# Kernel optimization log

Hardware: AMD Instinct MI355X
Metric: run time of the kernel (lower is better)

The kernel has to match this reference:

```python
import jax, jax.numpy as jnp
import numpy as np

B = 2000           # number of events (segments)
N = 1_000_000      # total points (sum of num_points)
D_IN, H, D_OUT = 16, 256, 128
EPS = 1e-5


def _layer_norm(x, g, b):
    m = x.mean(-1, keepdims=True)
    v = x.var(-1, keepdims=True)
    return (x - m) * jax.lax.rsqrt(v + EPS) * g + b


def setup_inputs() -> dict:
    key = jax.random.key(0)
    ks = jax.random.split(key, 8)
    # ragged counts, all positive, summing exactly to N
    rng = np.random.default_rng(0)
    counts = np.full(B, N // B, dtype=np.int64)
    d = rng.integers(-400, 401, size=B // 2)
    counts[: B // 2] += d
    counts[B // 2 :] -= d
    assert counts.sum() == N and (counts > 0).all()
    z_t = jax.random.normal(ks[0], (N, D_IN), dtype=jnp.float32)
    def lin(k, fi, fo):
        return jax.random.normal(k, (fi, fo), dtype=jnp.float32) / np.sqrt(fi)
    return {
        "z_t": z_t,
        "W1": lin(ks[1], D_IN, H), "b1": jnp.zeros((H,), jnp.float32),
        "g1": jnp.ones((H,), jnp.float32), "be1": jnp.zeros((H,), jnp.float32),
        "W2": lin(ks[2], H, H), "b2": jnp.zeros((H,), jnp.float32),
        "g2": jnp.ones((H,), jnp.float32), "be2": jnp.zeros((H,), jnp.float32),
        "W3": lin(ks[3], H, D_OUT), "b3": jnp.zeros((D_OUT,), jnp.float32),
        "num_points": jnp.asarray(counts, dtype=jnp.int64),
    }


def reference(z_t, W1, b1, g1, be1, W2, b2, g2, be2, W3, b3, num_points):
    # per-point phi MLP: Linear -> LN -> ReLU (x2) -> Linear
    h = jax.nn.relu(_layer_norm(z_t @ W1 + b1, g1, be1))
    h = jax.nn.relu(_layer_norm(h @ W2 + b2, g2, be2))
    phi = h @ W3 + b3                                  # [N, D_OUT]
    # fused ragged mean-pool + broadcast back (replaces split/stack/repeat_interleave)
    seg = jnp.repeat(jnp.arange(B), num_points, total_repeat_length=N)  # [N]
    sums = jax.ops.segment_sum(phi, seg, num_segments=B)                # [B, D_OUT]
    emb = sums / num_points[:, None].astype(phi.dtype)                  # mean pooling
    return emb[seg]                                                     # [N, D_OUT]
```

## Files before the change

kernel.cpp:

```cpp
#include <hip/hip_runtime.h>
#include <hip/hip_bf16.h>
#include <cstdint>
#include <cstddef>

#define NPTS  1000000
#define BSEG  2000
#define DIN   16
#define HDIM  256
#define DOUT  128
#define NTILE (NPTS / 32)
#define NWG   512

typedef __bf16          bf16x8 __attribute__((ext_vector_type(8)));
typedef unsigned short  us16x8 __attribute__((ext_vector_type(8)));
typedef unsigned int    u32x4  __attribute__((ext_vector_type(4)));
typedef float           f32x4  __attribute__((ext_vector_type(4)));

static __device__ __forceinline__ unsigned short f2bf(float x) {
    unsigned int u = __float_as_uint(x);
    u += 0x7fffu + ((u >> 16) & 1u);
    return (unsigned short)(u >> 16);
}

static __device__ __forceinline__ bf16x8 ldb8(const unsigned short* p) {
    u32x4 v = *(const u32x4*)p;
    return __builtin_bit_cast(bf16x8, v);
}
static __device__ __forceinline__ f32x4 mfma16(bf16x8 a, bf16x8 b, f32x4 c) {
    return __builtin_amdgcn_mfma_f32_16x16x32_bf16(a, b, c, 0, 0, 0);
}
static __device__ __forceinline__ void keep(bf16x8& v) {
    u32x4 u = __builtin_bit_cast(u32x4, v);
    unsigned a0 = u[0], a1 = u[1], a2 = u[2], a3 = u[3];
    asm volatile("" : "+v"(a0), "+v"(a1), "+v"(a2), "+v"(a3));
    u32x4 r; r[0] = a0; r[1] = a1; r[2] = a2; r[3] = a3;
    v = __builtin_bit_cast(bf16x8, r);
}

static __device__ __forceinline__ float rsum16(float x) {
    x += __builtin_bit_cast(float, __builtin_amdgcn_update_dpp(
             0, __builtin_bit_cast(int, x), 0x128, 0xf, 0xf, false));
    x += __builtin_bit_cast(float, __builtin_amdgcn_update_dpp(
             0, __builtin_bit_cast(int, x), 0x124, 0xf, 0xf, false));
    x += __builtin_bit_cast(float, __builtin_amdgcn_update_dpp(
             0, __builtin_bit_cast(int, x), 0x122, 0xf, 0xf, false));
    x += __builtin_bit_cast(float, __builtin_amdgcn_update_dpp(
             0, __builtin_bit_cast(int, x), 0x121, 0xf, 0xf, false));
    return x;
}

__global__ __launch_bounds__(1024) void scan_counts(const int* __restrict__ counts,
                                                    int* __restrict__ offsets) {
    __shared__ int a[2048];
    const int t = threadIdx.x;
    a[t]        = (t        < BSEG) ? counts[t]        : 0;
    a[t + 1024] = (t + 1024 < BSEG) ? counts[t + 1024] : 0;
    for (int s = 1; s < 2048; s <<= 1) {
        __syncthreads();
        int x1 = (t >= s) ? a[t - s] : 0;
        int x2 = a[t + 1024 - s];
        __syncthreads();
        a[t] += x1;
        a[t + 1024] += x2;
    }
    __syncthreads();
    if (t == 0) offsets[0] = 0;
    offsets[t + 1] = a[t];
    if (t + 1024 < BSEG) offsets[t + 1025] = a[t + 1024];
}

__global__ __launch_bounds__(256) void fill_seg(const int* __restrict__ offsets,
                                                unsigned short* __restrict__ seg) {
    const int b  = blockIdx.x;
    const int lo = offsets[b], hi = offsets[b + 1];
    for (int i = lo + threadIdx.x; i < hi; i += 256) seg[i] = (unsigned short)b;
}

__global__ __launch_bounds__(256) void prep_weights(const float* __restrict__ W1,
                                                    const float* __restrict__ W2,
                                                    unsigned short* __restrict__ w1t,
                                                    unsigned short* __restrict__ w2t) {
    const int i = blockIdx.x * 256 + threadIdx.x;
    if (i < HDIM * 32) {
        int n = i >> 5, k = i & 31;
        w1t[i] = (k < DIN) ? f2bf(W1[k * HDIM + n]) : (unsigned short)0;
    } else {
        int j = i - HDIM * 32;
        if (j < HDIM * HDIM) {
            int n = j >> 8, k = j & 255;
            w2t[j] = f2bf(W2[k * HDIM + n]);
        }
    }
}

__global__ __launch_bounds__(256, 2) void fused_phi_pool(
    const float* __restrict__ z,
    const unsigned short* __restrict__ w1t,
    const unsigned short* __restrict__ w2t,
    const float* __restrict__ b1, const float* __restrict__ g1, const float* __restrict__ be1,
    const float* __restrict__ b2, const float* __restrict__ g2, const float* __restrict__ be2,
    const unsigned short* __restrict__ seg,
    float* __restrict__ sums_h) {
    __shared__ __align__(16) unsigned short h1[32][264];
    __shared__ __align__(16) float part[2][32][8];
    __shared__ __align__(16) int seg_sm[2][32];

    const int tid  = threadIdx.x;
    const int wave = tid >> 6;
    const int lane = tid & 63;
    const int l15  = lane & 15;
    const int quad = lane >> 4;
    const int colw = wave * 64 + l15;
    const bool zlane = (quad < 2);

    bf16x8 bw1[4];
    bf16x8 bw2[4][8];
#pragma unroll
    for (int t = 0; t < 4; ++t) {
        const int n = (wave * 4 + t) * 16 + l15;
        bw1[t] = ldb8(w1t + n * 32 + quad * 8);
        keep(bw1[t]);
#pragma unroll
        for (int ks = 0; ks < 8; ++ks) {
            bw2[t][ks] = ldb8(w2t + n * 256 + ks * 32 + quad * 8);
            keep(bw2[t][ks]);
        }
    }
    float b1v[4], g1v[4], e1v[4], b2v[4], g2v[4], e2v[4];
#pragma unroll
    for (int t = 0; t < 4; ++t) {
        const int c = colw + t * 16;
        b1v[t] = b1[c]; g1v[t] = g1[c]; e1v[t] = be1[c];
        b2v[t] = b2[c]; g2v[t] = g2[c]; e2v[t] = be2[c];
    }

    float4 zn[2][2];
    {
        const int base0 = blockIdx.x * 32;
        if (zlane) {
#pragma unroll
            for (int mb = 0; mb < 2; ++mb) {
                const float* zp = z + (size_t)(base0 + mb * 16 + l15) * DIN + quad * 8;
                zn[mb][0] = *(const float4*)zp;
                zn[mb][1] = *(const float4*)(zp + 4);
            }
        }
    }

    int p = 0;
    for (int tile = blockIdx.x; tile < NTILE; tile += NWG, p ^= 1) {
        const int base = tile * 32;
        if (tid < 32) seg_sm[p][tid] = (int)seg[base + tid];

        float4 zc[2][2];
#pragma unroll
        for (int mb = 0; mb < 2; ++mb) { zc[mb][0] = zn[mb][0]; zc[mb][1] = zn[mb][1]; }
        const int ntile = tile + NWG;
        if (zlane && ntile < NTILE) {
            const int nb = ntile * 32;
#pragma unroll
            for (int mb = 0; mb < 2; ++mb) {
                const float* zp = z + (size_t)(nb + mb * 16 + l15) * DIN + quad * 8;
                zn[mb][0] = *(const float4*)zp;
                zn[mb][1] = *(const float4*)(zp + 4);
            }
        }

        f32x4 a1[2][4];
#pragma unroll
        for (int mb = 0; mb < 2; ++mb) {
            bf16x8 af;
            if (zlane) {
                us16x8 u;
                u[0] = f2bf(zc[mb][0].x); u[1] = f2bf(zc[mb][0].y);
                u[2] = f2bf(zc[mb][0].z); u[3] = f2bf(zc[mb][0].w);
                u[4] = f2bf(zc[mb][1].x); u[5] = f2bf(zc[mb][1].y);
                u[6] = f2bf(zc[mb][1].z); u[7] = f2bf(zc[mb][1].w);
                af = __builtin_bit_cast(bf16x8, u);
            } else {
                us16x8 u = {0, 0, 0, 0, 0, 0, 0, 0};
                af = __builtin_bit_cast(bf16x8, u);
            }
            const f32x4 zero = {0.f, 0.f, 0.f, 0.f};
#pragma unroll
            for (int t = 0; t < 4; ++t) a1[mb][t] = mfma16(af, bw1[t], zero);
        }
#pragma unroll
        for (int mb = 0; mb < 2; ++mb) {
            float s[4], q[4];
#pragma unroll
            for (int r = 0; r < 4; ++r) {
                float sv = 0.f, qv = 0.f;
#pragma unroll
                for (int t = 0; t < 4; ++t) {
                    float y = a1[mb][t][r] + b1v[t];
                    a1[mb][t][r] = y;
                    sv += y; qv += y * y;
                }
                s[r] = rsum16(sv); q[r] = rsum16(qv);
            }
            if (l15 == 0) {
#pragma unroll
                for (int r = 0; r < 4; ++r)
                    *(float2*)&part[p][mb * 16 + quad * 4 + r][wave * 2] =
                        make_float2(s[r], q[r]);
            }
        }
        __syncthreads();
#pragma unroll
        for (int mb = 0; mb < 2; ++mb) {
#pragma unroll
            for (int r = 0; r < 4; ++r) {
                const int row = mb * 16 + quad * 4 + r;
                float4 pa = *(const float4*)&part[p][row][0];
                float4 pb = *(const float4*)&part[p][row][4];
                float st = pa.x + pa.z + pb.x + pb.z;
                float qt = pa.y + pa.w + pb.y + pb.w;
                float mean = st * (1.f / 256.f);
                float var  = qt * (1.f / 256.f) - mean * mean;
                float rs   = rsqrtf(fmaxf(var, 0.f) + 1e-5f);
#pragma unroll
                for (int t = 0; t < 4; ++t) {
                    float A = rs * g1v[t];
                    float y = fmaxf(fmaf(a1[mb][t][r], A, fmaf(-mean, A, e1v[t])), 0.f);
                    h1[row][colw + t * 16] = f2bf(y);
                }
            }
        }
        __syncthreads();

        f32x4 a2[2][4];
#pragma unroll
        for (int mb = 0; mb < 2; ++mb) {
            const f32x4 zero = {0.f, 0.f, 0.f, 0.f};
#pragma unroll
            for (int t = 0; t < 4; ++t) a2[mb][t] = zero;
#pragma unroll
            for (int ks = 0; ks < 8; ++ks) {
                bf16x8 af = ldb8(&h1[mb * 16 + l15][ks * 32 + quad * 8]);
#pragma unroll
                for (int t = 0; t < 4; ++t) a2[mb][t] = mfma16(af, bw2[t][ks], a2[mb][t]);
            }
        }
#pragma unroll
        for (int mb = 0; mb < 2; ++mb) {
            float s[4], q[4];
#pragma unroll
            for (int r = 0; r < 4; ++r) {
                float sv = 0.f, qv = 0.f;
#pragma unroll
                for (int t = 0; t < 4; ++t) {
                    float y = a2[mb][t][r] + b2v[t];
                    a2[mb][t][r] = y;
                    sv += y; qv += y * y;
                }
                s[r] = rsum16(sv); q[r] = rsum16(qv);
            }
            if (l15 == 0) {
#pragma unroll
                for (int r = 0; r < 4; ++r)
                    *(float2*)&part[p][mb * 16 + quad * 4 + r][wave * 2] =
                        make_float2(s[r], q[r]);
            }
        }
        __syncthreads();
#pragma unroll
        for (int mb = 0; mb < 2; ++mb) {
#pragma unroll
            for (int r = 0; r < 4; ++r) {
                const int row = mb * 16 + quad * 4 + r;
                float4 pa = *(const float4*)&part[p][row][0];
                float4 pb = *(const float4*)&part[p][row][4];
                float st = pa.x + pa.z + pb.x + pb.z;
                float qt = pa.y + pa.w + pb.y + pb.w;
                float mean = st * (1.f / 256.f);
                float var  = qt * (1.f / 256.f) - mean * mean;
                float rs   = rsqrtf(fmaxf(var, 0.f) + 1e-5f);
#pragma unroll
                for (int t = 0; t < 4; ++t) {
                    float A = rs * g2v[t];
                    a2[mb][t][r] =
                        fmaxf(fmaf(a2[mb][t][r], A, fmaf(-mean, A, e2v[t])), 0.f);
                }
            }
        }

        const int s0  = seg_sm[p][0];
        const int s31 = seg_sm[p][31];
        if (s0 == s31) {
#pragma unroll
            for (int t = 0; t < 4; ++t) {
                float cs = a2[0][t][0] + a2[0][t][1] + a2[0][t][2] + a2[0][t][3]
                         + a2[1][t][0] + a2[1][t][1] + a2[1][t][2] + a2[1][t][3];
                cs += __shfl_xor(cs, 16, 64);
                cs += __shfl_xor(cs, 32, 64);
                if (quad == 0)
                    atomicAdd(&sums_h[s0 * HDIM + colw + t * 16], cs);
            }
        } else {
            const int* sgp = &seg_sm[p][0];
            float m0[4], m1[4];
#pragma unroll
            for (int r = 0; r < 4; ++r) {
                m0[r] = (sgp[quad * 4 + r]      == s0) ? 1.f : 0.f;
                m1[r] = (sgp[16 + quad * 4 + r] == s0) ? 1.f : 0.f;
            }
#pragma unroll
            for (int t = 0; t < 4; ++t) {
                float cs = 0.f, ca = 0.f;
#pragma unroll
                for (int r = 0; r < 4; ++r) {
                    cs += a2[0][t][r] + a2[1][t][r];
                    ca = fmaf(a2[0][t][r], m0[r], ca);
                    ca = fmaf(a2[1][t][r], m1[r], ca);
                }
                cs += __shfl_xor(cs, 16, 64);
                cs += __shfl_xor(cs, 32, 64);
                ca += __shfl_xor(ca, 16, 64);
                ca += __shfl_xor(ca, 32, 64);
                if (quad == 0) {
                    atomicAdd(&sums_h[s0  * HDIM + colw + t * 16], ca);
                    atomicAdd(&sums_h[s31 * HDIM + colw + t * 16], cs - ca);
                }
            }
        }
    }
}

__global__ __launch_bounds__(256) void emb_gemm(const float* __restrict__ sums_h,
                                                const float* __restrict__ W3,
                                                const float* __restrict__ b3,
                                                const int* __restrict__ counts,
                                                float* __restrict__ emb) {
    const int b = blockIdx.x * 2 + (threadIdx.x >> 7);
    const int o = threadIdx.x & 127;
    const float* sh = sums_h + b * HDIM;
    float acc = 0.f;
#pragma unroll 8
    for (int k = 0; k < HDIM; ++k) acc = fmaf(sh[k], W3[k * DOUT + o], acc);
    emb[b * DOUT + o] = acc / (float)counts[b] + b3[o];
}

__global__ __launch_bounds__(256) void broadcast_out(const float* __restrict__ emb,
                                                     const unsigned short* __restrict__ seg,
                                                     float* __restrict__ out) {
    const int idx = blockIdx.x * 256 + threadIdx.x;
    const int n = idx >> 4, oct = idx & 15;
    const int s = seg[n];
    float4 v0 = ((const float4*)emb)[s * 32 + oct * 2];
    float4 v1 = ((const float4*)emb)[s * 32 + oct * 2 + 1];
    ((float4*)out)[idx * 2]     = v0;
    ((float4*)out)[idx * 2 + 1] = v1;
}

extern "C" void kernel_launch(void* const* d_in, const int* in_sizes, int n_in,
                              void* d_out, int out_size, void* d_ws, size_t ws_size,
                              hipStream_t stream) {
    const float* z   = (const float*)d_in[0];
    const float* W1  = (const float*)d_in[1];
    const float* b1  = (const float*)d_in[2];
    const float* g1  = (const float*)d_in[3];
    const float* be1 = (const float*)d_in[4];
    const float* W2  = (const float*)d_in[5];
    const float* b2  = (const float*)d_in[6];
    const float* g2  = (const float*)d_in[7];
    const float* be2 = (const float*)d_in[8];
    const float* W3  = (const float*)d_in[9];
    const float* b3  = (const float*)d_in[10];
    const int* counts = (const int*)d_in[11];
    float* out = (float*)d_out;

    char* ws = (char*)d_ws;
    float*          sums_h  = (float*)(ws);
    float*          emb     = (float*)(ws + 2048000);
    int*            offsets = (int*)  (ws + 3072000);
    unsigned short* seg     = (unsigned short*)(ws + 3080016);
    unsigned short* w1t     = (unsigned short*)(ws + 5080016);
    unsigned short* w2t     = (unsigned short*)(ws + 5096400);

    hipMemsetAsync(sums_h, 0, (size_t)BSEG * HDIM * sizeof(float), stream);
    scan_counts<<<1, 1024, 0, stream>>>(counts, offsets);
    fill_seg<<<BSEG, 256, 0, stream>>>(offsets, seg);
    prep_weights<<<(HDIM * 32 + HDIM * HDIM) / 256, 256, 0, stream>>>(W1, W2, w1t, w2t);
    fused_phi_pool<<<NWG, 256, 0, stream>>>(z, w1t, w2t,
                                            b1, g1, be1, b2, g2, be2,
                                            seg, sums_h);
    emb_gemm<<<BSEG / 2, 256, 0, stream>>>(sums_h, W3, b3, counts, emb);
    broadcast_out<<<NPTS * 16 / 256, 256, 0, stream>>>(emb, seg, out);
}
```

Measured before the change: 1.032 ms.

## Split fused MLP across eight waves and prefetch z into LDS asynchronously

```diff
diff --git a/kernel.cpp b/kernel.cpp
--- a/kernel.cpp
+++ b/kernel.cpp
@@ -35,6 +35,12 @@
     asm volatile("" : "+v"(a0), "+v"(a1), "+v"(a2), "+v"(a3));
     u32x4 r; r[0] = a0; r[1] = a1; r[2] = a2; r[3] = a3;
     v = __builtin_bit_cast(bf16x8, r);
+}
+
+static __device__ __forceinline__ void async16(const float* g, float* l) {
+    __builtin_amdgcn_global_load_lds(
+        (const __attribute__((address_space(1))) void*)g,
+        (__attribute__((address_space(3))) void*)l, 16, 0, 0);
 }
 
 static __device__ __forceinline__ float rsum16(float x) {
@@ -93,7 +99,7 @@
     }
 }
 
-__global__ __launch_bounds__(256, 2) void fused_phi_pool(
+__global__ __launch_bounds__(512, 4) void fused_phi_pool(
     const float* __restrict__ z,
     const unsigned short* __restrict__ w1t,
     const unsigned short* __restrict__ w2t,
@@ -102,22 +108,22 @@
     const unsigned short* __restrict__ seg,
     float* __restrict__ sums_h) {
     __shared__ __align__(16) unsigned short h1[32][264];
-    __shared__ __align__(16) float part[2][32][8];
-    __shared__ __align__(16) int seg_sm[2][32];
+    __shared__ __align__(16) float part[2][32][16];
+    __shared__ __align__(16) float z_lds[2][32][16];
+    __shared__ __align__(16) int   seg_sm[2][32];
 
     const int tid  = threadIdx.x;
     const int wave = tid >> 6;
     const int lane = tid & 63;
     const int l15  = lane & 15;
     const int quad = lane >> 4;
-    const int colw = wave * 64 + l15;
-    const bool zlane = (quad < 2);
-
-    bf16x8 bw1[4];
-    bf16x8 bw2[4][8];
-#pragma unroll
-    for (int t = 0; t < 4; ++t) {
-        const int n = (wave * 4 + t) * 16 + l15;
+    const bool zl  = (quad < 2);
+
+    bf16x8 bw1[2];
+    bf16x8 bw2[2][8];
+#pragma unroll
+    for (int t = 0; t < 2; ++t) {
+        const int n = wave * 32 + t * 16 + l15;
         bw1[t] = ldb8(w1t + n * 32 + quad * 8);
         keep(bw1[t]);
 #pragma unroll
@@ -126,56 +132,43 @@
             keep(bw2[t][ks]);
         }
     }
-    float b1v[4], g1v[4], e1v[4], b2v[4], g2v[4], e2v[4];
-#pragma unroll
-    for (int t = 0; t < 4; ++t) {
-        const int c = colw + t * 16;
+    float b1v[2], g1v[2], e1v[2], b2v[2], g2v[2], e2v[2];
+#pragma unroll
+    for (int t = 0; t < 2; ++t) {
+        const int c = wave * 32 + t * 16 + l15;
         b1v[t] = b1[c]; g1v[t] = g1[c]; e1v[t] = be1[c];
         b2v[t] = b2[c]; g2v[t] = g2[c]; e2v[t] = be2[c];
     }
 
-    float4 zn[2][2];
-    {
-        const int base0 = blockIdx.x * 32;
-        if (zlane) {
-#pragma unroll
-            for (int mb = 0; mb < 2; ++mb) {
-                const float* zp = z + (size_t)(base0 + mb * 16 + l15) * DIN + quad * 8;
-                zn[mb][0] = *(const float4*)zp;
-                zn[mb][1] = *(const float4*)(zp + 4);
-            }
-        }
-    }
+    if (wave == 0) {
+        const float* gp = z + (size_t)blockIdx.x * 512 + lane * 4;
+        async16(gp,       &z_lds[0][0][0]);
+        async16(gp + 256, &z_lds[0][16][0]);
+    }
+    asm volatile("s_waitcnt vmcnt(0)");
+    __syncthreads();
 
     int p = 0;
     for (int tile = blockIdx.x; tile < NTILE; tile += NWG, p ^= 1) {
-        const int base = tile * 32;
-        if (tid < 32) seg_sm[p][tid] = (int)seg[base + tid];
-
-        float4 zc[2][2];
-#pragma unroll
-        for (int mb = 0; mb < 2; ++mb) { zc[mb][0] = zn[mb][0]; zc[mb][1] = zn[mb][1]; }
+        if (tid < 32) seg_sm[p][tid] = (int)seg[tile * 32 + tid];
+
         const int ntile = tile + NWG;
-        if (zlane && ntile < NTILE) {
-            const int nb = ntile * 32;
-#pragma unroll
-            for (int mb = 0; mb < 2; ++mb) {
-                const float* zp = z + (size_t)(nb + mb * 16 + l15) * DIN + quad * 8;
-                zn[mb][0] = *(const float4*)zp;
-                zn[mb][1] = *(const float4*)(zp + 4);
-            }
-        }
-
-        f32x4 a1[2][4];
+        if (wave == 0 && ntile < NTILE) {
+            const float* gp = z + (size_t)ntile * 512 + lane * 4;
+            async16(gp,       &z_lds[p ^ 1][0][0]);
+            async16(gp + 256, &z_lds[p ^ 1][16][0]);
+        }
+
+        f32x4 a1[2][2];
 #pragma unroll
         for (int mb = 0; mb < 2; ++mb) {
             bf16x8 af;
-            if (zlane) {
+            if (zl) {
+                f32x4 v0 = *(const f32x4*)&z_lds[p][mb * 16 + l15][quad * 8];
+                f32x4 v1 = *(const f32x4*)&z_lds[p][mb * 16 + l15][quad * 8 + 4];
                 us16x8 u;
-                u[0] = f2bf(zc[mb][0].x); u[1] = f2bf(zc[mb][0].y);
-                u[2] = f2bf(zc[mb][0].z); u[3] = f2bf(zc[mb][0].w);
-                u[4] = f2bf(zc[mb][1].x); u[5] = f2bf(zc[mb][1].y);
-                u[6] = f2bf(zc[mb][1].z); u[7] = f2bf(zc[mb][1].w);
+                u[0] = f2bf(v0[0]); u[1] = f2bf(v0[1]); u[2] = f2bf(v0[2]); u[3] = f2bf(v0[3]);
+                u[4] = f2bf(v1[0]); u[5] = f2bf(v1[1]); u[6] = f2bf(v1[2]); u[7] = f2bf(v1[3]);
                 af = __builtin_bit_cast(bf16x8, u);
             } else {
                 us16x8 u = {0, 0, 0, 0, 0, 0, 0, 0};
@@ -183,27 +176,20 @@
             }
             const f32x4 zero = {0.f, 0.f, 0.f, 0.f};
 #pragma unroll
-            for (int t = 0; t < 4; ++t) a1[mb][t] = mfma16(af, bw1[t], zero);
-        }
-#pragma unroll
-        for (int mb = 0; mb < 2; ++mb) {
-            float s[4], q[4];
-#pragma unroll
-            for (int r = 0; r < 4; ++r) {
-                float sv = 0.f, qv = 0.f;
-#pragma unroll
-                for (int t = 0; t < 4; ++t) {
-                    float y = a1[mb][t][r] + b1v[t];
-                    a1[mb][t][r] = y;
-                    sv += y; qv += y * y;
-                }
-                s[r] = rsum16(sv); q[r] = rsum16(qv);
-            }
-            if (l15 == 0) {
-#pragma unroll
-                for (int r = 0; r < 4; ++r)
+            for (int t = 0; t < 2; ++t) a1[mb][t] = mfma16(af, bw1[t], zero);
+        }
+#pragma unroll
+        for (int mb = 0; mb < 2; ++mb) {
+#pragma unroll
+            for (int r = 0; r < 4; ++r) {
+                float y0 = a1[mb][0][r] + b1v[0];
+                float y1 = a1[mb][1][r] + b1v[1];
+                a1[mb][0][r] = y0; a1[mb][1][r] = y1;
+                float sv = rsum16(y0 + y1);
+                float qv = rsum16(y0 * y0 + y1 * y1);
+                if (l15 == 0)
                     *(float2*)&part[p][mb * 16 + quad * 4 + r][wave * 2] =
-                        make_float2(s[r], q[r]);
+                        make_float2(sv, qv);
             }
         }
         __syncthreads();
@@ -212,55 +198,50 @@
 #pragma unroll
             for (int r = 0; r < 4; ++r) {
                 const int row = mb * 16 + quad * 4 + r;
-                float4 pa = *(const float4*)&part[p][row][0];
-                float4 pb = *(const float4*)&part[p][row][4];
-                float st = pa.x + pa.z + pb.x + pb.z;
-                float qt = pa.y + pa.w + pb.y + pb.w;
+                const float* pr = &part[p][row][0];
+                float4 pa = *(const float4*)(pr);
+                float4 pb = *(const float4*)(pr + 4);
+                float4 pc = *(const float4*)(pr + 8);
+                float4 pd = *(const float4*)(pr + 12);
+                float st = (pa.x + pa.z) + (pb.x + pb.z) + (pc.x + pc.z) + (pd.x + pd.z);
+                float qt = (pa.y + pa.w) + (pb.y + pb.w) + (pc.y + pc.w) + (pd.y + pd.w);
                 float mean = st * (1.f / 256.f);
                 float var  = qt * (1.f / 256.f) - mean * mean;
                 float rs   = rsqrtf(fmaxf(var, 0.f) + 1e-5f);
 #pragma unroll
-                for (int t = 0; t < 4; ++t) {
+                for (int t = 0; t < 2; ++t) {
                     float A = rs * g1v[t];
                     float y = fmaxf(fmaf(a1[mb][t][r], A, fmaf(-mean, A, e1v[t])), 0.f);
-                    h1[row][colw + t * 16] = f2bf(y);
+                    h1[row][wave * 32 + t * 16 + l15] = f2bf(y);
                 }
             }
         }
         __syncthreads();
 
-        f32x4 a2[2][4];
+        f32x4 a2[2][2];
 #pragma unroll
         for (int mb = 0; mb < 2; ++mb) {
             const f32x4 zero = {0.f, 0.f, 0.f, 0.f};
-#pragma unroll
-            for (int t = 0; t < 4; ++t) a2[mb][t] = zero;
+            a2[mb][0] = zero; a2[mb][1] = zero;
 #pragma unroll
             for (int ks = 0; ks < 8; ++ks) {
                 bf16x8 af = ldb8(&h1[mb * 16 + l15][ks * 32 + quad * 8]);
 #pragma unroll
-                for (int t = 0; t < 4; ++t) a2[mb][t] = mfma16(af, bw2[t][ks], a2[mb][t]);
-            }
-        }
-#pragma unroll
-        for (int mb = 0; mb < 2; ++mb) {
-            float s[4], q[4];
-#pragma unroll
-            for (int r = 0; r < 4; ++r) {
-                float sv = 0.f, qv = 0.f;
-#pragma unroll
-                for (int t = 0; t < 4; ++t) {
-                    float y = a2[mb][t][r] + b2v[t];
-                    a2[mb][t][r] = y;
-                    sv += y; qv += y * y;
-                }
-                s[r] = rsum16(sv); q[r] = rsum16(qv);
-            }
-            if (l15 == 0) {
-#pragma unroll
-                for (int r = 0; r < 4; ++r)
+                for (int t = 0; t < 2; ++t) a2[mb][t] = mfma16(af, bw2[t][ks], a2[mb][t]);
+            }
+        }
+#pragma unroll
+        for (int mb = 0; mb < 2; ++mb) {
+#pragma unroll
+            for (int r = 0; r < 4; ++r) {
+                float y0 = a2[mb][0][r] + b2v[0];
+                float y1 = a2[mb][1][r] + b2v[1];
+                a2[mb][0][r] = y0; a2[mb][1][r] = y1;
+                float sv = rsum16(y0 + y1);
+                float qv = rsum16(y0 * y0 + y1 * y1);
+                if (l15 == 0)
                     *(float2*)&part[p][mb * 16 + quad * 4 + r][wave * 2] =
-                        make_float2(s[r], q[r]);
+                        make_float2(sv, qv);
             }
         }
         __syncthreads();
@@ -269,15 +250,18 @@
 #pragma unroll
             for (int r = 0; r < 4; ++r) {
                 const int row = mb * 16 + quad * 4 + r;
-                float4 pa = *(const float4*)&part[p][row][0];
-                float4 pb = *(const float4*)&part[p][row][4];
-                float st = pa.x + pa.z + pb.x + pb.z;
-                float qt = pa.y + pa.w + pb.y + pb.w;
+                const float* pr = &part[p][row][0];
+                float4 pa = *(const float4*)(pr);
+                float4 pb = *(const float4*)(pr + 4);
+                float4 pc = *(const float4*)(pr + 8);
+                float4 pd = *(const float4*)(pr + 12);
+                float st = (pa.x + pa.z) + (pb.x + pb.z) + (pc.x + pc.z) + (pd.x + pd.z);
+                float qt = (pa.y + pa.w) + (pb.y + pb.w) + (pc.y + pc.w) + (pd.y + pd.w);
                 float mean = st * (1.f / 256.f);
                 float var  = qt * (1.f / 256.f) - mean * mean;
                 float rs   = rsqrtf(fmaxf(var, 0.f) + 1e-5f);
 #pragma unroll
-                for (int t = 0; t < 4; ++t) {
+                for (int t = 0; t < 2; ++t) {
                     float A = rs * g2v[t];
                     a2[mb][t][r] =
                         fmaxf(fmaf(a2[mb][t][r], A, fmaf(-mean, A, e2v[t])), 0.f);
@@ -289,13 +273,13 @@
         const int s31 = seg_sm[p][31];
         if (s0 == s31) {
 #pragma unroll
-            for (int t = 0; t < 4; ++t) {
+            for (int t = 0; t < 2; ++t) {
                 float cs = a2[0][t][0] + a2[0][t][1] + a2[0][t][2] + a2[0][t][3]
                          + a2[1][t][0] + a2[1][t][1] + a2[1][t][2] + a2[1][t][3];
                 cs += __shfl_xor(cs, 16, 64);
                 cs += __shfl_xor(cs, 32, 64);
                 if (quad == 0)
-                    atomicAdd(&sums_h[s0 * HDIM + colw + t * 16], cs);
+                    atomicAdd(&sums_h[s0 * HDIM + wave * 32 + t * 16 + l15], cs);
             }
         } else {
             const int* sgp = &seg_sm[p][0];
@@ -306,7 +290,7 @@
                 m1[r] = (sgp[16 + quad * 4 + r] == s0) ? 1.f : 0.f;
             }
 #pragma unroll
-            for (int t = 0; t < 4; ++t) {
+            for (int t = 0; t < 2; ++t) {
                 float cs = 0.f, ca = 0.f;
 #pragma unroll
                 for (int r = 0; r < 4; ++r) {
@@ -319,8 +303,9 @@
                 ca += __shfl_xor(ca, 16, 64);
                 ca += __shfl_xor(ca, 32, 64);
                 if (quad == 0) {
-                    atomicAdd(&sums_h[s0  * HDIM + colw + t * 16], ca);
-                    atomicAdd(&sums_h[s31 * HDIM + colw + t * 16], cs - ca);
+                    const int c = wave * 32 + t * 16 + l15;
+                    atomicAdd(&sums_h[s0  * HDIM + c], ca);
+                    atomicAdd(&sums_h[s31 * HDIM + c], cs - ca);
                 }
             }
         }
@@ -347,10 +332,11 @@
     const int idx = blockIdx.x * 256 + threadIdx.x;
     const int n = idx >> 4, oct = idx & 15;
     const int s = seg[n];
-    float4 v0 = ((const float4*)emb)[s * 32 + oct * 2];
-    float4 v1 = ((const float4*)emb)[s * 32 + oct * 2 + 1];
-    ((float4*)out)[idx * 2]     = v0;
-    ((float4*)out)[idx * 2 + 1] = v1;
+    const f32x4* ev = (const f32x4*)emb;
+    f32x4 v0 = ev[s * 32 + oct * 2];
+    f32x4 v1 = ev[s * 32 + oct * 2 + 1];
+    __builtin_nontemporal_store(v0, (f32x4*)out + idx * 2);
+    __builtin_nontemporal_store(v1, (f32x4*)out + idx * 2 + 1);
 }
 
 extern "C" void kernel_launch(void* const* d_in, const int* in_sizes, int n_in,
@@ -382,7 +368,7 @@
     scan_counts<<<1, 1024, 0, stream>>>(counts, offsets);
     fill_seg<<<BSEG, 256, 0, stream>>>(offsets, seg);
     prep_weights<<<(HDIM * 32 + HDIM * HDIM) / 256, 256, 0, stream>>>(W1, W2, w1t, w2t);
-    fused_phi_pool<<<NWG, 256, 0, stream>>>(z, w1t, w2t,
+    fused_phi_pool<<<NWG, 512, 0, stream>>>(z, w1t, w2t,
                                             b1, g1, be1, b2, g2, be2,
                                             seg, sums_h);
     emb_gemm<<<BSEG / 2, 256, 0, stream>>>(sums_h, W3, b3, counts, emb);
```

New measurement: 1.284 ms. 24.4% more time.
